# Optimization experiments

Measured on AMD Instinct MI355X. Metric: run time of the kernel, lower is better.

Reference implementation:

```python
import jax, jax.numpy as jnp
import numpy as np

B, H, HKV, S, D = 1, 32, 4, 2048, 128
NEG = -1e9  # causal mask fill (float32-safe, like torch finfo.min in spirit)


def setup_inputs() -> dict:
    key = jax.random.key(0)
    kq, kk, kv, ks = jax.random.split(key, 4)
    query = jax.random.normal(kq, (B, H, S, D), dtype=jnp.float32)
    k = jax.random.normal(kk, (B, HKV, S, D), dtype=jnp.float32)
    v = jax.random.normal(kv, (B, HKV, S, D), dtype=jnp.float32)
    sinks = jax.random.normal(ks, (H,), dtype=jnp.float32)
    # causal additive mask [B, 1, S, S]
    causal = jnp.where(jnp.tril(jnp.ones((S, S), dtype=bool)), 0.0, NEG).astype(jnp.float32)
    attention_mask = jnp.broadcast_to(causal[None, None], (B, 1, S, S))
    return {"query": query, "key": k, "value": v,
            "attention_mask": attention_mask, "sinks": sinks}


def reference(query, key, value, attention_mask, sinks):
    scaling = 1.0 / jnp.sqrt(jnp.asarray(D, dtype=query.dtype))
    groups = H // HKV
    # repeat_kv: [B, HKV, S, D] -> [B, H, S, D]
    k = jnp.repeat(key, groups, axis=1)
    v = jnp.repeat(value, groups, axis=1)
    # scores [B, H, S, S]
    attn = jnp.einsum('bhqd,bhkd->bhqk', query, k) * scaling
    attn = attn + attention_mask[:, :, :, :attn.shape[-1]]
    # append per-head sink column -> [B, H, S, S+1]
    sink_col = jnp.broadcast_to(sinks.reshape(1, H, 1, 1), (B, H, S, 1)).astype(attn.dtype)
    combined = jnp.concatenate([attn, sink_col], axis=-1)
    combined = combined - jnp.max(combined, axis=-1, keepdims=True)
    probs = jax.nn.softmax(combined, axis=-1)[..., :-1]
    # PV matmul, then [B, H, S, D] -> [B, S, H, D]
    out = jnp.einsum('bhqk,bhkd->bhqd', probs, v)
    return jnp.transpose(out, (0, 2, 1, 3))
```

## Files before the change

### kernel.cpp

```cpp
#include <hip/hip_runtime.h>
#include <hip/hip_bf16.h>

#define NH   32
#define SEQ  2048
#define HD   128
#define QBLK 64
#define KVB  64
#define NQT  (SEQ / QBLK)
#define NUNITS (NQT * NH)
#define TILE_ELEMS (KVB * HD)
#define TILE_BYTES 16384

typedef __attribute__((ext_vector_type(8))) short bf16x8;
typedef __attribute__((ext_vector_type(4))) float f32x4;
typedef __attribute__((ext_vector_type(2))) unsigned int u32x2;

#define VMCNT0 asm volatile("s_waitcnt vmcnt(0)" ::: "memory")

static __device__ __forceinline__ unsigned short f2bf(float f) {
  __hip_bfloat16 h = __float2bfloat16(f);
  union { __hip_bfloat16 h; unsigned short u; } c; c.h = h;
  return c.u;
}

__device__ __forceinline__ int swzK(int row, int colByte) {
  return row * 256 + (colByte ^ ((row & 7) << 4));
}
__device__ __forceinline__ int swzV(int d, int kvByte) {
  return d * 128 + (kvByte ^ ((d & 7) << 4));
}
__device__ __forceinline__ int swzP(int row, int colByte) {
  return row * 128 + (colByte ^ ((row & 7) << 4));
}

__global__ __launch_bounds__(256)
void convert_kv(const float* __restrict__ K, const float* __restrict__ V,
                unsigned short* __restrict__ Ki, unsigned short* __restrict__ Vi)
{
  const int b = blockIdx.x;
  const float* Ks = K + (size_t)b * TILE_ELEMS;
  const float* Vs = V + (size_t)b * TILE_ELEMS;
  char* ki = (char*)(Ki + (size_t)b * TILE_ELEMS);
  char* vi = (char*)(Vi + (size_t)b * TILE_ELEMS);
  const int tid  = threadIdx.x;
  const int srow = tid >> 4;
  const int scol = (tid & 15) * 8;
  #pragma unroll
  for (int i = 0; i < 4; ++i) {
    const int row = i * 16 + srow;
    float tk[8], tv[8];
    *(f32x4*)(tk)     = *(const f32x4*)(Ks + row * HD + scol);
    *(f32x4*)(tk + 4) = *(const f32x4*)(Ks + row * HD + scol + 4);
    *(f32x4*)(tv)     = *(const f32x4*)(Vs + row * HD + scol);
    *(f32x4*)(tv + 4) = *(const f32x4*)(Vs + row * HD + scol + 4);
    bf16x8 k8;
    #pragma unroll
    for (int j = 0; j < 8; ++j) k8[j] = (short)f2bf(tk[j]);
    *(bf16x8*)(ki + swzK(row, scol * 2)) = k8;
    #pragma unroll
    for (int j = 0; j < 8; ++j)
      *(unsigned short*)(vi + swzV(scol + j, row * 2)) = f2bf(tv[j]);
  }
}

__device__ __forceinline__ void stage_tile(const unsigned short* img, char* lds, int tid) {
  #pragma unroll
  for (int k = 0; k < 4; ++k)
    __builtin_amdgcn_global_load_lds((const unsigned int*)((const char*)img + k * 4096 + tid * 16),
                                     (unsigned int*)(lds + k * 4096 + tid * 16), 16, 0, 0);
}

__global__ __launch_bounds__(256, 4)
void attn_fwd(const float* __restrict__ Q, const float* __restrict__ sinks,
              const unsigned short* __restrict__ Kimg, const unsigned short* __restrict__ Vimg,
              float* __restrict__ out, int* __restrict__ counter)
{
  __shared__ __align__(16) char Kl[2][TILE_BYTES];
  __shared__ __align__(16) char Vl[2][TILE_BYTES];
  __shared__ __align__(16) char Pl[4][2048];
  __shared__ int sh_unit;

  const int tid  = threadIdx.x;
  const int lane = tid & 63;
  const int w    = tid >> 6;
  const int lr   = lane & 15;
  const int lg   = lane >> 4;

  const float QSC = 0.08838834764831845f * 1.4426950408889634f;
  const float EC  = 17.312340490667562f;

  bf16x8 ones;
  #pragma unroll
  for (int i = 0; i < 8; ++i) ones[i] = (short)0x3F80;
  char* pw = Pl[w];

  for (;;) {
    if (tid == 0) sh_unit = atomicAdd(counter, 1);
    __syncthreads();
    const int u = sh_unit;
    if (u >= NUNITS) break;

    const int qt  = (NQT - 1) - (u >> 5);
    const int h   = u & 31;
    const int kvh = h >> 3;
    const int q0  = qt * QBLK;
    const int nt  = qt + 1;

    const unsigned short* Kt = Kimg + (size_t)(kvh * 32) * TILE_ELEMS;
    const unsigned short* Vt = Vimg + (size_t)(kvh * 32) * TILE_ELEMS;

    stage_tile(Kt, Kl[0], tid);
    stage_tile(Vt, Vl[0], tid);

    const int qb   = q0 + w * 16;
    const int qmax = qb + 15;
    const int qme  = qb + lr;

    bf16x8 qa[4];
    {
      const float* qp = Q + (size_t)(h * SEQ + qb + lr) * HD + lg * 8;
      #pragma unroll
      for (int ks = 0; ks < 4; ++ks) {
        float t0[8];
        *(f32x4*)(t0)     = *(const f32x4*)(qp + ks * 32);
        *(f32x4*)(t0 + 4) = *(const f32x4*)(qp + ks * 32 + 4);
        bf16x8 qv;
        #pragma unroll
        for (int jj = 0; jj < 8; ++jj) qv[jj] = (short)f2bf(t0[jj] * QSC);
        qa[ks] = qv;
      }
    }

    f32x4 acc[8];
    f32x4 accl = (f32x4){0.f, 0.f, 0.f, 0.f};
    #pragma unroll
    for (int i = 0; i < 8; ++i) acc[i] = (f32x4){0.f, 0.f, 0.f, 0.f};

    for (int i = 0; i < nt; ++i) {
      VMCNT0;
      __syncthreads();
      if (i + 1 < nt) {
        stage_tile(Kt + (size_t)(i + 1) * TILE_ELEMS, Kl[(i + 1) & 1], tid);
        stage_tile(Vt + (size_t)(i + 1) * TILE_ELEMS, Vl[(i + 1) & 1], tid);
      }

      const int kv0 = i * KVB;
      if (kv0 > qmax) continue;
      const char* kb = Kl[i & 1];
      const char* vb = Vl[i & 1];

      f32x4 sc[4];
      __builtin_amdgcn_s_setprio(1);
      #pragma unroll
      for (int cb = 0; cb < 4; ++cb) {
        f32x4 a = (f32x4){0.f, 0.f, 0.f, 0.f};
        #pragma unroll
        for (int ks = 0; ks < 4; ++ks) {
          bf16x8 kf = *(const bf16x8*)(kb + swzK(cb * 16 + lr, (ks * 32 + lg * 8) * 2));
          a = __builtin_amdgcn_mfma_f32_16x16x32_bf16(kf, qa[ks], a, 0, 0, 0);
        }
        sc[cb] = a;
      }
      __builtin_amdgcn_s_setprio(0);

      #pragma unroll
      for (int cb = 0; cb < 4; ++cb) {
        float p[4];
        #pragma unroll
        for (int r = 0; r < 4; ++r) {
          const int kv = kv0 + cb * 16 + lg * 4 + r;
          float e = __builtin_amdgcn_exp2f(sc[cb][r] - EC);
          p[r] = (kv > qme) ? 0.f : e;
        }
        u32x2 wd;
        wd[0] = (unsigned int)f2bf(p[0]) | ((unsigned int)f2bf(p[1]) << 16);
        wd[1] = (unsigned int)f2bf(p[2]) | ((unsigned int)f2bf(p[3]) << 16);
        *(u32x2*)(pw + swzP(lr, cb * 32 + lg * 8)) = wd;
      }

      bf16x8 pa[2];
      #pragma unroll
      for (int h2 = 0; h2 < 2; ++h2)
        pa[h2] = *(const bf16x8*)(pw + swzP(lr, h2 * 64 + lg * 16));

      accl = __builtin_amdgcn_mfma_f32_16x16x32_bf16(pa[0], ones, accl, 0, 0, 0);
      accl = __builtin_amdgcn_mfma_f32_16x16x32_bf16(pa[1], ones, accl, 0, 0, 0);
      __builtin_amdgcn_s_setprio(1);
      #pragma unroll
      for (int ncb = 0; ncb < 8; ++ncb) {
        bf16x8 vf0 = *(const bf16x8*)(vb + swzV(ncb * 16 + lr, lg * 16));
        bf16x8 vf1 = *(const bf16x8*)(vb + swzV(ncb * 16 + lr, 64 + lg * 16));
        acc[ncb] = __builtin_amdgcn_mfma_f32_16x16x32_bf16(pa[0], vf0, acc[ncb], 0, 0, 0);
        acc[ncb] = __builtin_amdgcn_mfma_f32_16x16x32_bf16(pa[1], vf1, acc[ncb], 0, 0, 0);
      }
      __builtin_amdgcn_s_setprio(0);
    }

    const float sk = sinks[h];
    const float sadd = __builtin_amdgcn_exp2f(sk * 1.4426950408889634f - EC);
    #pragma unroll
    for (int r = 0; r < 4; ++r) {
      const float rd = 1.0f / (accl[r] + sadd);
      const size_t q = qb + lg * 4 + r;
      float* op = out + (q * NH + h) * HD + lr;
      #pragma unroll
      for (int ncb = 0; ncb < 8; ++ncb)
        op[ncb * 16] = acc[ncb][r] * rd;
    }
  }
}

extern "C" void kernel_launch(void* const* d_in, const int* in_sizes, int n_in,
                              void* d_out, int out_size, void* d_ws, size_t ws_size,
                              hipStream_t stream) {
  const float* Q     = (const float*)d_in[0];
  const float* K     = (const float*)d_in[1];
  const float* V     = (const float*)d_in[2];
  const float* sinks = (const float*)d_in[4];
  float* out = (float*)d_out;

  unsigned short* Kimg = (unsigned short*)d_ws;
  unsigned short* Vimg = Kimg + (size_t)128 * TILE_ELEMS;
  int* counter = (int*)((char*)d_ws + (size_t)8 * 1024 * 1024 / 2);

  hipMemsetAsync(counter, 0, 64, stream);
  convert_kv<<<dim3(128), 256, 0, stream>>>(K, V, Kimg, Vimg);
  attn_fwd<<<dim3(512), 256, 0, stream>>>(Q, sinks, Kimg, Vimg, out, counter);
}
```

Measured before the change: 86.32 us.

## Rewrite attention as per-wave 32x32 MFMA tiles reading K/V directly from global

Replaces the block-level LDS double-buffered K/V staging with per-wave work units of 32 query rows. Each wave loads K and V fragments straight from a pre-swizzled global image and uses 32x32x16 bf16 MFMAs. P is moved into A-operand layout with permlane32 swaps instead of an LDS round trip. Row sums are accumulated in registers instead of via an extra ones-MFMA, causal masking is applied only on the diagonal tile, and output is transposed through LDS for coalesced stores. This removes block-wide barriers and shared K/V traffic, at the cost of lost K/V reuse across waves (more L2 traffic) and lower occupancy (launch bounds go from 4 to 2).

```diff
diff --git a/kernel.cpp b/kernel.cpp
--- a/kernel.cpp
+++ b/kernel.cpp
@@ -1,211 +1,204 @@
 #include <hip/hip_runtime.h>
 #include <hip/hip_bf16.h>
 
-#define NH   32
-#define SEQ  2048
-#define HD   128
-#define QBLK 64
-#define KVB  64
-#define NQT  (SEQ / QBLK)
-#define NUNITS (NQT * NH)
-#define TILE_ELEMS (KVB * HD)
-#define TILE_BYTES 16384
-
-typedef __attribute__((ext_vector_type(8))) short bf16x8;
-typedef __attribute__((ext_vector_type(4))) float f32x4;
-typedef __attribute__((ext_vector_type(2))) unsigned int u32x2;
-
-#define VMCNT0 asm volatile("s_waitcnt vmcnt(0)" ::: "memory")
+#define NH    32
+#define SEQ   2048
+#define HD    128
+#define QW    32
+#define KVB   64
+#define NRANK 64
+#define NUNITS (NRANK * NH)
+#define KTILE  16384
+#define KVHB   (32 * KTILE)
+
+typedef __attribute__((ext_vector_type(8)))  short bf16x8;
+typedef __attribute__((ext_vector_type(4)))  float f32x4;
+typedef __attribute__((ext_vector_type(16))) float f32x16;
+
+#define LGKM0 asm volatile("s_waitcnt lgkmcnt(0)" ::: "memory")
 
 static __device__ __forceinline__ unsigned short f2bf(float f) {
   __hip_bfloat16 h = __float2bfloat16(f);
   union { __hip_bfloat16 h; unsigned short u; } c; c.h = h;
   return c.u;
 }
-
-__device__ __forceinline__ int swzK(int row, int colByte) {
-  return row * 256 + (colByte ^ ((row & 7) << 4));
-}
-__device__ __forceinline__ int swzV(int d, int kvByte) {
-  return d * 128 + (kvByte ^ ((d & 7) << 4));
-}
-__device__ __forceinline__ int swzP(int row, int colByte) {
-  return row * 128 + (colByte ^ ((row & 7) << 4));
+static __device__ __forceinline__ unsigned int pk2(float a, float b) {
+  return (unsigned int)f2bf(a) | ((unsigned int)f2bf(b) << 16);
+}
+static __device__ __forceinline__ bf16x8 mk8(unsigned int w0, unsigned int w1,
+                                             unsigned int w2, unsigned int w3) {
+  union { unsigned int w[4]; bf16x8 v; } t;
+  t.w[0] = w0; t.w[1] = w1; t.w[2] = w2; t.w[3] = w3; return t.v;
 }
 
 __global__ __launch_bounds__(256)
 void convert_kv(const float* __restrict__ K, const float* __restrict__ V,
-                unsigned short* __restrict__ Ki, unsigned short* __restrict__ Vi)
+                char* __restrict__ Ki, char* __restrict__ Vi)
 {
   const int b = blockIdx.x;
-  const float* Ks = K + (size_t)b * TILE_ELEMS;
-  const float* Vs = V + (size_t)b * TILE_ELEMS;
-  char* ki = (char*)(Ki + (size_t)b * TILE_ELEMS);
-  char* vi = (char*)(Vi + (size_t)b * TILE_ELEMS);
-  const int tid  = threadIdx.x;
-  const int srow = tid >> 4;
-  const int scol = (tid & 15) * 8;
+  const float* Ks = K + (size_t)b * (KVB * HD);
+  const float* Vs = V + (size_t)b * (KVB * HD);
+  char* kt = Ki + (size_t)b * KTILE;
+  char* vt = Vi + (size_t)b * KTILE;
+  const int tid   = threadIdx.x;
+  const int r16   = tid >> 4;
+  const int dcol  = (tid & 15) * 8;
+  const int dstep = dcol >> 4;
+  const int h2d   = (dcol >> 3) & 1;
   #pragma unroll
   for (int i = 0; i < 4; ++i) {
-    const int row = i * 16 + srow;
+    const int row = i * 16 + r16;
     float tk[8], tv[8];
-    *(f32x4*)(tk)     = *(const f32x4*)(Ks + row * HD + scol);
-    *(f32x4*)(tk + 4) = *(const f32x4*)(Ks + row * HD + scol + 4);
-    *(f32x4*)(tv)     = *(const f32x4*)(Vs + row * HD + scol);
-    *(f32x4*)(tv + 4) = *(const f32x4*)(Vs + row * HD + scol + 4);
+    *(f32x4*)(tk)     = *(const f32x4*)(Ks + row * HD + dcol);
+    *(f32x4*)(tk + 4) = *(const f32x4*)(Ks + row * HD + dcol + 4);
+    *(f32x4*)(tv)     = *(const f32x4*)(Vs + row * HD + dcol);
+    *(f32x4*)(tv + 4) = *(const f32x4*)(Vs + row * HD + dcol + 4);
     bf16x8 k8;
     #pragma unroll
     for (int j = 0; j < 8; ++j) k8[j] = (short)f2bf(tk[j]);
-    *(bf16x8*)(ki + swzK(row, scol * 2)) = k8;
-    #pragma unroll
-    for (int j = 0; j < 8; ++j)
-      *(unsigned short*)(vi + swzV(scol + j, row * 2)) = f2bf(tv[j]);
+    *(bf16x8*)(kt + ((row >> 5) * 8 + dstep) * 1024 + (h2d * 32 + (row & 31)) * 16) = k8;
+    const int s = (row >> 4) & 3, h2v = (row >> 3) & 1, jv = row & 7;
+    #pragma unroll
+    for (int j = 0; j < 8; ++j) {
+      const int d = dcol + j;
+      *(unsigned short*)(vt + ((d >> 5) * 4 + s) * 1024 + (h2v * 32 + (d & 31)) * 16 + jv * 2)
+        = f2bf(tv[j]);
+    }
   }
 }
 
-__device__ __forceinline__ void stage_tile(const unsigned short* img, char* lds, int tid) {
-  #pragma unroll
-  for (int k = 0; k < 4; ++k)
-    __builtin_amdgcn_global_load_lds((const unsigned int*)((const char*)img + k * 4096 + tid * 16),
-                                     (unsigned int*)(lds + k * 4096 + tid * 16), 16, 0, 0);
-}
-
-__global__ __launch_bounds__(256, 4)
+__global__ __launch_bounds__(256, 2)
 void attn_fwd(const float* __restrict__ Q, const float* __restrict__ sinks,
-              const unsigned short* __restrict__ Kimg, const unsigned short* __restrict__ Vimg,
+              const char* __restrict__ Ki, const char* __restrict__ Vi,
               float* __restrict__ out, int* __restrict__ counter)
 {
-  __shared__ __align__(16) char Kl[2][TILE_BYTES];
-  __shared__ __align__(16) char Vl[2][TILE_BYTES];
-  __shared__ __align__(16) char Pl[4][2048];
-  __shared__ int sh_unit;
+  __shared__ __align__(16) char Ol[4][4096];
 
   const int tid  = threadIdx.x;
   const int lane = tid & 63;
   const int w    = tid >> 6;
-  const int lr   = lane & 15;
-  const int lg   = lane >> 4;
+  const int lq   = lane & 31;
+  const int hi   = lane >> 5;
+  char* ow = Ol[w];
 
   const float QSC = 0.08838834764831845f * 1.4426950408889634f;
   const float EC  = 17.312340490667562f;
 
-  bf16x8 ones;
-  #pragma unroll
-  for (int i = 0; i < 8; ++i) ones[i] = (short)0x3F80;
-  char* pw = Pl[w];
-
   for (;;) {
-    if (tid == 0) sh_unit = atomicAdd(counter, 1);
-    __syncthreads();
-    const int u = sh_unit;
+    int u = 0;
+    if (lane == 0) u = atomicAdd(counter, 1);
+    u = __shfl(u, 0);
     if (u >= NUNITS) break;
 
-    const int qt  = (NQT - 1) - (u >> 5);
-    const int h   = u & 31;
-    const int kvh = h >> 3;
-    const int q0  = qt * QBLK;
-    const int nt  = qt + 1;
-
-    const unsigned short* Kt = Kimg + (size_t)(kvh * 32) * TILE_ELEMS;
-    const unsigned short* Vt = Vimg + (size_t)(kvh * 32) * TILE_ELEMS;
-
-    stage_tile(Kt, Kl[0], tid);
-    stage_tile(Vt, Vl[0], tid);
-
-    const int qb   = q0 + w * 16;
-    const int qmax = qb + 15;
-    const int qme  = qb + lr;
-
-    bf16x8 qa[4];
+    const int k2   = u >> 1;
+    const int h    = k2 & 31;
+    const int rank = k2 >> 5;
+    const int qt   = (u & 1) ? rank : (63 - rank);
+    const int q0   = qt * QW;
+    const int nt   = (qt >> 1) + 1;
+    const int kvh  = h >> 3;
+    const int qme  = q0 + lq;
+
+    const char* kp = Ki + (size_t)kvh * KVHB;
+    const char* vp = Vi + (size_t)kvh * KVHB;
+
+    bf16x8 qf[8];
     {
-      const float* qp = Q + (size_t)(h * SEQ + qb + lr) * HD + lg * 8;
-      #pragma unroll
-      for (int ks = 0; ks < 4; ++ks) {
+      const float* qp = Q + ((size_t)h * SEQ + qme) * HD + hi * 8;
+      #pragma unroll
+      for (int dstep = 0; dstep < 8; ++dstep) {
         float t0[8];
-        *(f32x4*)(t0)     = *(const f32x4*)(qp + ks * 32);
-        *(f32x4*)(t0 + 4) = *(const f32x4*)(qp + ks * 32 + 4);
+        *(f32x4*)(t0)     = *(const f32x4*)(qp + dstep * 16);
+        *(f32x4*)(t0 + 4) = *(const f32x4*)(qp + dstep * 16 + 4);
         bf16x8 qv;
         #pragma unroll
-        for (int jj = 0; jj < 8; ++jj) qv[jj] = (short)f2bf(t0[jj] * QSC);
-        qa[ks] = qv;
-      }
-    }
-
-    f32x4 acc[8];
-    f32x4 accl = (f32x4){0.f, 0.f, 0.f, 0.f};
-    #pragma unroll
-    for (int i = 0; i < 8; ++i) acc[i] = (f32x4){0.f, 0.f, 0.f, 0.f};
+        for (int j = 0; j < 8; ++j) qv[j] = (short)f2bf(t0[j] * QSC);
+        qf[dstep] = qv;
+      }
+    }
+
+    f32x16 acc[4];
+    #pragma unroll
+    for (int d = 0; d < 4; ++d)
+      acc[d] = (f32x16){0.f,0.f,0.f,0.f,0.f,0.f,0.f,0.f,0.f,0.f,0.f,0.f,0.f,0.f,0.f,0.f};
+    float lsum = 0.f;
 
     for (int i = 0; i < nt; ++i) {
-      VMCNT0;
-      __syncthreads();
-      if (i + 1 < nt) {
-        stage_tile(Kt + (size_t)(i + 1) * TILE_ELEMS, Kl[(i + 1) & 1], tid);
-        stage_tile(Vt + (size_t)(i + 1) * TILE_ELEMS, Vl[(i + 1) & 1], tid);
-      }
-
-      const int kv0 = i * KVB;
-      if (kv0 > qmax) continue;
-      const char* kb = Kl[i & 1];
-      const char* vb = Vl[i & 1];
-
-      f32x4 sc[4];
-      __builtin_amdgcn_s_setprio(1);
-      #pragma unroll
-      for (int cb = 0; cb < 4; ++cb) {
-        f32x4 a = (f32x4){0.f, 0.f, 0.f, 0.f};
-        #pragma unroll
-        for (int ks = 0; ks < 4; ++ks) {
-          bf16x8 kf = *(const bf16x8*)(kb + swzK(cb * 16 + lr, (ks * 32 + lg * 8) * 2));
-          a = __builtin_amdgcn_mfma_f32_16x16x32_bf16(kf, qa[ks], a, 0, 0, 0);
+      const char* ktile = kp + (size_t)i * KTILE + lane * 16;
+      const char* vtile = vp + (size_t)i * KTILE + lane * 16;
+      const bool diag = (i == nt - 1);
+      bf16x8 pf[4];
+
+      #pragma unroll
+      for (int kvb = 0; kvb < 2; ++kvb) {
+        f32x16 sc = (f32x16){0.f,0.f,0.f,0.f,0.f,0.f,0.f,0.f,0.f,0.f,0.f,0.f,0.f,0.f,0.f,0.f};
+        #pragma unroll
+        for (int dstep = 0; dstep < 8; ++dstep) {
+          bf16x8 kf = *(const bf16x8*)(ktile + (kvb * 8 + dstep) * 1024);
+          sc = __builtin_amdgcn_mfma_f32_32x32x16_bf16(kf, qf[dstep], sc, 0, 0, 0);
         }
-        sc[cb] = a;
-      }
-      __builtin_amdgcn_s_setprio(0);
-
-      #pragma unroll
-      for (int cb = 0; cb < 4; ++cb) {
-        float p[4];
-        #pragma unroll
-        for (int r = 0; r < 4; ++r) {
-          const int kv = kv0 + cb * 16 + lg * 4 + r;
-          float e = __builtin_amdgcn_exp2f(sc[cb][r] - EC);
-          p[r] = (kv > qme) ? 0.f : e;
+
+        float p[16];
+        #pragma unroll
+        for (int r = 0; r < 16; ++r)
+          p[r] = __builtin_amdgcn_exp2f(sc[r] - EC);
+        if (diag) {
+          const int kvbase = i * KVB + kvb * 32 + 4 * hi;
+          #pragma unroll
+          for (int r = 0; r < 16; ++r) {
+            const int kv = kvbase + (r & 3) + 8 * (r >> 2);
+            if (kv > qme) p[r] = 0.f;
+          }
         }
-        u32x2 wd;
-        wd[0] = (unsigned int)f2bf(p[0]) | ((unsigned int)f2bf(p[1]) << 16);
-        wd[1] = (unsigned int)f2bf(p[2]) | ((unsigned int)f2bf(p[3]) << 16);
-        *(u32x2*)(pw + swzP(lr, cb * 32 + lg * 8)) = wd;
-      }
-
-      bf16x8 pa[2];
-      #pragma unroll
-      for (int h2 = 0; h2 < 2; ++h2)
-        pa[h2] = *(const bf16x8*)(pw + swzP(lr, h2 * 64 + lg * 16));
-
-      accl = __builtin_amdgcn_mfma_f32_16x16x32_bf16(pa[0], ones, accl, 0, 0, 0);
-      accl = __builtin_amdgcn_mfma_f32_16x16x32_bf16(pa[1], ones, accl, 0, 0, 0);
-      __builtin_amdgcn_s_setprio(1);
-      #pragma unroll
-      for (int ncb = 0; ncb < 8; ++ncb) {
-        bf16x8 vf0 = *(const bf16x8*)(vb + swzV(ncb * 16 + lr, lg * 16));
-        bf16x8 vf1 = *(const bf16x8*)(vb + swzV(ncb * 16 + lr, 64 + lg * 16));
-        acc[ncb] = __builtin_amdgcn_mfma_f32_16x16x32_bf16(pa[0], vf0, acc[ncb], 0, 0, 0);
-        acc[ncb] = __builtin_amdgcn_mfma_f32_16x16x32_bf16(pa[1], vf1, acc[ncb], 0, 0, 0);
-      }
-      __builtin_amdgcn_s_setprio(0);
-    }
-
-    const float sk = sinks[h];
-    const float sadd = __builtin_amdgcn_exp2f(sk * 1.4426950408889634f - EC);
-    #pragma unroll
-    for (int r = 0; r < 4; ++r) {
-      const float rd = 1.0f / (accl[r] + sadd);
-      const size_t q = qb + lg * 4 + r;
-      float* op = out + (q * NH + h) * HD + lr;
-      #pragma unroll
-      for (int ncb = 0; ncb < 8; ++ncb)
-        op[ncb * 16] = acc[ncb][r] * rd;
+        #pragma unroll
+        for (int r = 0; r < 16; ++r) lsum += p[r];
+
+        unsigned int X0 = pk2(p[0],  p[1]),  X1 = pk2(p[2],  p[3]);
+        unsigned int Y0 = pk2(p[4],  p[5]),  Y1 = pk2(p[6],  p[7]);
+        unsigned int Z0 = pk2(p[8],  p[9]),  Z1 = pk2(p[10], p[11]);
+        unsigned int W0 = pk2(p[12], p[13]), W1 = pk2(p[14], p[15]);
+        asm volatile("v_permlane32_swap_b32 %0, %1" : "+v"(X0), "+v"(Y0));
+        asm volatile("v_permlane32_swap_b32 %0, %1" : "+v"(X1), "+v"(Y1));
+        asm volatile("v_permlane32_swap_b32 %0, %1" : "+v"(Z0), "+v"(W0));
+        asm volatile("v_permlane32_swap_b32 %0, %1" : "+v"(Z1), "+v"(W1));
+        pf[kvb * 2 + 0] = mk8(X0, X1, Y0, Y1);
+        pf[kvb * 2 + 1] = mk8(Z0, Z1, W0, W1);
+      }
+
+      #pragma unroll
+      for (int dblk = 0; dblk < 4; ++dblk) {
+        #pragma unroll
+        for (int s = 0; s < 4; ++s) {
+          bf16x8 vf = *(const bf16x8*)(vtile + (dblk * 4 + s) * 1024);
+          acc[dblk] = __builtin_amdgcn_mfma_f32_32x32x16_bf16(vf, pf[s], acc[dblk], 0, 0, 0);
+        }
+      }
+    }
+
+    lsum += __shfl_xor(lsum, 32);
+    const float sadd = __builtin_amdgcn_exp2f(sinks[h] * 1.4426950408889634f - EC);
+    const float rd = 1.0f / (lsum + sadd);
+
+    const int qrow = lane >> 1;
+    const int half = lane & 1;
+    const int sx   = qrow & 7;
+    #pragma unroll
+    for (int dblk = 0; dblk < 4; ++dblk) {
+      #pragma unroll
+      for (int m = 0; m < 4; ++m) {
+        f32x4 t;
+        #pragma unroll
+        for (int e = 0; e < 4; ++e) t[e] = acc[dblk][4 * m + e] * rd;
+        *(f32x4*)(ow + lq * 128 + ((m * 32 + hi * 16) ^ ((lq & 7) << 4))) = t;
+      }
+      LGKM0;
+      float* og = out + (((size_t)(q0 + qrow)) * NH + h) * HD + dblk * 32 + half * 16;
+      #pragma unroll
+      for (int c = 0; c < 4; ++c) {
+        f32x4 t = *(const f32x4*)(ow + qrow * 128 + (((half * 4 + c) ^ sx) * 16));
+        *(f32x4*)(og + c * 4) = t;
+      }
+      LGKM0;
     }
   }
 }
@@ -219,11 +212,11 @@
   const float* sinks = (const float*)d_in[4];
   float* out = (float*)d_out;
 
-  unsigned short* Kimg = (unsigned short*)d_ws;
-  unsigned short* Vimg = Kimg + (size_t)128 * TILE_ELEMS;
-  int* counter = (int*)((char*)d_ws + (size_t)8 * 1024 * 1024 / 2);
+  char* Ki = (char*)d_ws;
+  char* Vi = Ki + (size_t)4 * KVHB;
+  int* counter = (int*)(Vi + (size_t)4 * KVHB);
 
   hipMemsetAsync(counter, 0, 64, stream);
-  convert_kv<<<dim3(128), 256, 0, stream>>>(K, V, Kimg, Vimg);
-  attn_fwd<<<dim3(512), 256, 0, stream>>>(Q, sinks, Kimg, Vimg, out, counter);
-}
+  convert_kv<<<dim3(128), 256, 0, stream>>>(K, V, Ki, Vi);
+  attn_fwd<<<dim3(512), 256, 0, stream>>>(Q, sinks, Ki, Vi, out, counter);
+}
```

Result: slower. 188.8 us (+118.7%).
